# Kernel tuning notes

Hardware: AMD Instinct MI355X
Metric: run time of the kernel (lower is better)

## Reference

```python
import jax, jax.numpy as jnp
import numpy as np
from jax import lax

GEN_POLY = ("1111001", "1011011")  # rate 1/2, constraint length 7 (octal 171/133)


def build_trellis(gen_poly):
    """Feed-forward (non-recursive) convolutional trellis tables.

    State = shift-register contents, most-recent bit is the MSB of the state
    index. Returns int32 tables, each [ns, ni]:
      to_nodes[s, b]        : next state from state s with input bit b
      op_by_fromnode[s, b]  : emitted output-symbol index for (s, b)
      from_nodes[j, m]      : m-th predecessor state of state j
      ip_by_tonode[j, m]    : input bit taken on that predecessor transition
    """
    mu = len(gen_poly[0]) - 1
    ns, ni = 2 ** mu, 2
    g = np.array([[int(c) for c in p] for p in gen_poly])  # [conv_n, mu+1]
    to_nodes = np.zeros((ns, ni), np.int32)
    op_by_fromnode = np.zeros((ns, ni), np.int32)
    from_nodes = np.zeros((ns, ni), np.int32)
    ip_by_tonode = np.zeros((ns, ni), np.int32)
    fill = np.zeros(ns, np.int32)
    for s in range(ns):
        rbits = [(s >> (mu - 1 - j)) & 1 for j in range(mu)]
        for b in range(ni):
            w = np.array([b] + rbits)                 # full window [b, r0..r_{mu-1}]
            obits = (g @ w) % 2                        # output bits, MSB first
            o = int("".join(str(int(x)) for x in obits), 2)
            j = int("".join(str(x) for x in ([b] + rbits[:-1])), 2)
            to_nodes[s, b] = j
            op_by_fromnode[s, b] = o
            from_nodes[j, fill[j]] = s
            ip_by_tonode[j, fill[j]] = b
            fill[j] += 1
    return to_nodes, op_by_fromnode, from_nodes, ip_by_tonode


TO_NODES, OP_BY_FROM, FROM_NODES, IP_BY_TO = build_trellis(GEN_POLY)
CONV_N = len(GEN_POLY)
MU = len(GEN_POLY[0]) - 1
NS = 2 ** MU
NO = 2 ** CONV_N
# output-symbol bit patterns, MSB first, mapped to signs (1-2*bit)
_OP_BITS = np.array([[(o >> (CONV_N - 1 - j)) & 1 for j in range(CONV_N)]
                     for o in range(NO)], np.float32)
OP_SIGN = jnp.asarray(1.0 - 2.0 * _OP_BITS)  # [NO, CONV_N]
IP_SIGN = jnp.asarray([1.0, -1.0])           # sign of input bit b: 1-2b


def setup_inputs() -> dict:
    key = jax.random.key(0)
    k1, k2 = jax.random.split(key)
    B, n = 256, 4096
    T = n // CONV_N  # = k = 2048 info bits
    llr_ch = jax.random.normal(k1, (B, n), dtype=jnp.float32)
    llr_a = jax.random.normal(k2, (B, T), dtype=jnp.float32)
    return {"llr_ch": llr_ch, "llr_a": llr_a}


def _bcjr(llr_ch, llr_a):
    B, n = llr_ch.shape
    T = n // CONV_N
    # branch metrics: bm[t, b, o] = exp(0.5 * sum_j llr[b, t, j] * (1-2*opbit_j(o)))
    llr_r = llr_ch.reshape(B, T, CONV_N)
    bm = jnp.exp(0.5 * jnp.einsum('btj,oj->tbo', llr_r, OP_SIGN))  # [T, B, NO]
    llr_a_t = llr_a.T  # [T, B]

    def gamma_fn(bm_t, la_t):
        # a-priori factor exp(0.5*llr_a*(1-2b)) times channel branch metric
        ap = jnp.exp(0.5 * la_t[:, None, None] * IP_SIGN[None, None, :])  # [B,1,2]
        return ap * bm_t[:, OP_BY_FROM]  # [B, NS, 2]

    alpha0 = jnp.zeros((B, NS), jnp.float32).at[:, 0].set(1.0)

    def fwd(alpha_prev, inp):
        bm_t, la_t = inp
        gam = gamma_fn(bm_t, la_t)                        # [B, NS, 2] by from-state
        ag = gam * alpha_prev[:, :, None]                  # alpha_{t} * gamma_t
        agt = ag[:, FROM_NODES, IP_BY_TO]                  # regroup by to-state
        alpha = agt.sum(-1)
        alpha = alpha / alpha.sum(-1, keepdims=True)       # normalize (as in TF code)
        return alpha, alpha_prev                            # emit alpha BEFORE step t

    _, alphas = lax.scan(fwd, alpha0, (bm, llr_a_t))       # alphas[t] = alpha_t, [T,B,NS]

    beta_T = jnp.full((B, NS), 1.0 / NS, jnp.float32)      # non-terminated: uniform

    def bwd(beta_next, inp):
        bm_t, la_t, alpha_t = inp
        gam = gamma_fn(bm_t, la_t)                         # [B, NS, 2]
        bg = gam * beta_next[:, TO_NODES]                  # gamma * beta_{t+1}(to)
        beta = bg.sum(-1)
        beta = beta / beta.sum(-1, keepdims=True)
        joint = alpha_t[:, :, None] * bg                   # APP per (state, bit)
        llr_t = jnp.log(joint[..., 0].sum(-1)) - jnp.log(joint[..., 1].sum(-1))
        return beta, llr_t

    _, llrs_rev = lax.scan(bwd, beta_T, (bm[::-1], llr_a_t[::-1], alphas[::-1]))
    return llrs_rev[::-1].T  # [B, T] soft LLRs (hard_out=False)


def reference(llr_ch, llr_a):
    return _bcjr(llr_ch, llr_a)
```

## Files before the change

### kernel.cpp

```cpp
#include <hip/hip_runtime.h>

#define T_LEN 2048
#define NSTATE 64
#define NCHUNK 16
#define CH_S 128
#define WARM 64
#define NCH_B 32
#define CH_B 64
#define RK 16

template <int CTRL>
__device__ __forceinline__ float dpp_add(float v) {
    int r = __builtin_amdgcn_update_dpp(0, __float_as_int(v), CTRL, 0xF, 0xF, true);
    return v + __int_as_float(r);
}
__device__ __forceinline__ float red63(float v) {
    v = dpp_add<0x111>(v);
    v = dpp_add<0x112>(v);
    v = dpp_add<0x114>(v);
    v = dpp_add<0x118>(v);
    v = dpp_add<0x142>(v);
    v = dpp_add<0x143>(v);
    return v;
}
__device__ __forceinline__ float red_half(float v) {
    v = dpp_add<0x111>(v);
    v = dpp_add<0x112>(v);
    v = dpp_add<0x114>(v);
    v = dpp_add<0x118>(v);
    v = dpp_add<0x142>(v);
    return v;
}
__device__ __forceinline__ float rdlane(float v, int l) {
    return __uint_as_float(__builtin_amdgcn_readlane(__float_as_uint(v), l));
}
__device__ __forceinline__ float bcast63(float v) { return rdlane(v, 63); }
__device__ __forceinline__ float pair_sum_xor1(float v) { return dpp_add<0xB1>(v); }
__device__ __forceinline__ unsigned short bf16_of(float f) {
    return (unsigned short)((__float_as_uint(f) + 0x8000u) >> 16);
}
__device__ __forceinline__ float bf16_lo(unsigned u) { return __uint_as_float(u << 16); }
__device__ __forceinline__ float bf16_hi(unsigned u) { return __uint_as_float(u & 0xffff0000u); }


__global__ __launch_bounds__(256, 8)
void bcjr_beta_kernel(const float* __restrict__ llr_ch,
                      const float* __restrict__ llr_a,
                      unsigned short* __restrict__ wsB)
{
    const int wave  = blockIdx.x * 4 + (threadIdx.x >> 6);
    const int lane  = threadIdx.x & 63;
    const int chunk = wave & (NCH_B - 1);
    const int b     = wave >> 5;

    const float c0 = 1.0f - 2.0f * (float)(__popc(lane & 57) & 1);
    const float c1 = 1.0f - 2.0f * (float)(__popc(lane & 27) & 1);
    const float kE = 0.5f * 1.442695040888963f;
    const float k0 = kE * c0, k1 = kE * c1;

    const float* chp = llr_ch + (size_t)b * (2 * T_LEN);
    const float* lap = llr_a  + (size_t)b * T_LEN;
    unsigned short* w = wsB + (size_t)b * T_LEN * NSTATE;

    const int bs0 = lane >> 1;
    const int bs1 = 32 + (lane >> 1);
    const int t0 = chunk * CH_B;
    const int te = (chunk == NCH_B - 1) ? (t0 + CH_B) : (t0 + CH_B + WARM);
    float state = 1.0f / 64.0f;

    for (int g = te - RK; g >= t0; g -= RK) {
        const bool store = (g < t0 + CH_B);
        #pragma unroll
        for (int h = 1; h >= 0; --h) {
            const int gb = g + 8 * h;
            const float4* c4 = (const float4*)(chp + 2 * gb);
            const float4* a4 = (const float4*)(lap + gb);
            float4 cc[4], aa[2];
            #pragma unroll
            for (int i = 0; i < 4; ++i) cc[i] = c4[i];
            #pragma unroll
            for (int i = 0; i < 2; ++i) aa[i] = a4[i];
            unsigned short* wb = w + (size_t)gb * NSTATE + lane;
            #pragma unroll
            for (int i = 7; i >= 0; --i) {
                float l0 = (i & 1) ? cc[i >> 1].z : cc[i >> 1].x;
                float l1 = (i & 1) ? cc[i >> 1].w : cc[i >> 1].y;
                float la = ((const float*)aa)[i];
                if (store) wb[i * NSTATE] = bf16_of(state);
                float x   = fmaf(la, kE, fmaf(l0, k0, l1 * k1));
                float g0v = exp2f(x);
                float g1v = __builtin_amdgcn_rcpf(g0v);
                float t0v = __shfl(state, bs0, 64);
                float t1v = __shfl(state, bs1, 64);
                state = fmaf(g0v, t0v, g1v * t1v);
            }
        }
        float s = bcast63(red63(state));
        state = state * __builtin_amdgcn_rcpf(s);
    }
}

__global__ __launch_bounds__(256, 4)
void bcjr_alpha_llr_kernel(const float* __restrict__ llr_ch,
                           const float* __restrict__ llr_a,
                           const unsigned short* __restrict__ wsB,
                           float* __restrict__ out)
{
    const int wave  = blockIdx.x * 4 + (threadIdx.x >> 6);
    const int lane  = threadIdx.x & 63;
    const int chunk = wave & (NCHUNK - 1);
    const int b     = wave >> 4;

    const float c0 = 1.0f - 2.0f * (float)(__popc(lane & 57) & 1);
    const float c1 = 1.0f - 2.0f * (float)(__popc(lane & 27) & 1);
    const float kE = 0.5f * 1.442695040888963f;
    const float k0 = kE * c0, k1 = kE * c1;
    const float LN2 = 0.69314718055994531f;

    const float* chp = llr_ch + (size_t)b * (2 * T_LEN);
    const float* lap = llr_a  + (size_t)b * T_LEN;
    float* outp      = out    + (size_t)b * T_LEN;

    const int  fs0 = 2 * (lane & 31);
    const bool fhi = (lane >= 32);
    const int t0 = chunk * CH_S;
    const int ts = (chunk == 0) ? t0 : t0 - WARM;
    float state = (chunk == 0) ? ((lane == 0) ? 1.0f : 0.0f) : (1.0f / 64.0f);

    for (int g = ts; g < t0; g += RK) {
        #pragma unroll
        for (int h = 0; h < 2; ++h) {
            const int gb = g + 8 * h;
            const float4* c4 = (const float4*)(chp + 2 * gb);
            const float4* a4 = (const float4*)(lap + gb);
            float4 cc[4], aa[2];
            #pragma unroll
            for (int i = 0; i < 4; ++i) cc[i] = c4[i];
            #pragma unroll
            for (int i = 0; i < 2; ++i) aa[i] = a4[i];
            #pragma unroll
            for (int i = 0; i < 8; ++i) {
                float l0 = (i & 1) ? cc[i >> 1].z : cc[i >> 1].x;
                float l1 = (i & 1) ? cc[i >> 1].w : cc[i >> 1].y;
                float la = ((const float*)aa)[i];
                float x   = fmaf(la, kE, fmaf(l0, k0, l1 * k1));
                float g0v = exp2f(x);
                float g1v = __builtin_amdgcn_rcpf(g0v);
                float s0  = pair_sum_xor1(state * g0v);
                float s1  = pair_sum_xor1(state * g1v);
                float a0  = __shfl(s0, fs0, 64);
                float a1  = __shfl(s1, fs0, 64);
                state = fhi ? a1 : a0;
            }
        }
        float s = bcast63(red63(state));
        state = state * __builtin_amdgcn_rcpf(s);
    }

    const unsigned* brow = (const unsigned*)(wsB + (size_t)b * T_LEN * NSTATE);
    const int  bdw = lane >> 1;
    const bool bhi = (lane & 1) != 0;
    float keep = 0.0f;

    for (int g = t0; g < t0 + CH_S; g += RK) {
        #pragma unroll
        for (int h = 0; h < 2; ++h) {
            const int gb = g + 8 * h;
            const float4* c4 = (const float4*)(chp + 2 * gb);
            const float4* a4 = (const float4*)(lap + gb);
            float4 cc[4], aa[2];
            #pragma unroll
            for (int i = 0; i < 4; ++i) cc[i] = c4[i];
            #pragma unroll
            for (int i = 0; i < 2; ++i) aa[i] = a4[i];
            unsigned bu[8];
            const unsigned* r = brow + (size_t)gb * 32;
            #pragma unroll
            for (int i = 0; i < 8; ++i) bu[i] = r[i * 32 + bdw];
            #pragma unroll
            for (int i = 0; i < 8; ++i) {
                const int t = gb + i;
                float l0 = (i & 1) ? cc[i >> 1].z : cc[i >> 1].x;
                float l1 = (i & 1) ? cc[i >> 1].w : cc[i >> 1].y;
                float la = ((const float*)aa)[i];
                float x   = fmaf(la, kE, fmaf(l0, k0, l1 * k1));
                float g0v = exp2f(x);
                float g1v = __builtin_amdgcn_rcpf(g0v);
                float ag0 = state * g0v;
                float ag1 = state * g1v;
                float s0  = pair_sum_xor1(ag0);
                float s1  = pair_sum_xor1(ag1);
                float a0  = __shfl(s0, fs0, 64);
                float a1  = __shfl(s1, fs0, 64);
                float an  = fhi ? a1 : a0;
                float bv  = bhi ? bf16_hi(bu[i]) : bf16_lo(bu[i]);
                float v   = red_half(an * bv);
                float n0  = rdlane(v, 31);
                float n1  = rdlane(v, 63);
                float llr = LN2 * (__log2f(n0) - __log2f(n1));
                keep = (lane == (t & 63)) ? llr : keep;
                state = an;
            }
        }
        if ((g & 63) == 48) outp[g - 48 + lane] = keep;
        float s = bcast63(red63(state));
        state = state * __builtin_amdgcn_rcpf(s);
    }
}

extern "C" void kernel_launch(void* const* d_in, const int* in_sizes, int n_in,
                              void* d_out, int out_size, void* d_ws, size_t ws_size,
                              hipStream_t stream) {
    const float* llr_ch = (const float*)d_in[0];
    const float* llr_a  = (const float*)d_in[1];
    float* out = (float*)d_out;
    unsigned short* wsB = (unsigned short*)d_ws;

    int B = in_sizes[0] / (2 * T_LEN);
    int nw_beta  = B * NCH_B;
    int nw_alpha = B * NCHUNK;
    hipLaunchKernelGGL(bcjr_beta_kernel, dim3(nw_beta / 4), dim3(256), 0, stream,
                       llr_ch, llr_a, wsB);
    hipLaunchKernelGGL(bcjr_alpha_llr_kernel, dim3(nw_alpha / 4), dim3(256), 0, stream,
                       llr_ch, llr_a, wsB, out);
}
```

Before: 142.2 us.

## Fuse beta and alpha/LLR passes into one kernel with beta in LDS

Replaces the two-kernel scheme (a beta pass writing bf16 betas to global workspace, then an alpha+LLR pass reading them back) with a single kernel. Each 128-thread block owns a 128-step chunk: two waves each compute betas for one 64-step half into shared memory, synchronise, then each runs the forward alpha recursion with warm-up and the LLR output for its half. This removes the global round-trip of the beta table and the second launch. The cost is more warm-up recursion per output step on the alpha side, 16 KB of LDS per block, and smaller blocks. The log-ratio is also computed as a single log of a ratio instead of two logs.

```diff
diff --git a/kernel.cpp b/kernel.cpp
--- a/kernel.cpp
+++ b/kernel.cpp
@@ -1,12 +1,10 @@
 #include <hip/hip_runtime.h>
 
 #define T_LEN 2048
-#define NSTATE 64
 #define NCHUNK 16
-#define CH_S 128
+#define CH 128
+#define HALF 64
 #define WARM 64
-#define NCH_B 32
-#define CH_B 64
 #define RK 16
 
 template <int CTRL>
@@ -39,77 +37,20 @@
 __device__ __forceinline__ unsigned short bf16_of(float f) {
     return (unsigned short)((__float_as_uint(f) + 0x8000u) >> 16);
 }
-__device__ __forceinline__ float bf16_lo(unsigned u) { return __uint_as_float(u << 16); }
-__device__ __forceinline__ float bf16_hi(unsigned u) { return __uint_as_float(u & 0xffff0000u); }
-
-
-__global__ __launch_bounds__(256, 8)
-void bcjr_beta_kernel(const float* __restrict__ llr_ch,
-                      const float* __restrict__ llr_a,
-                      unsigned short* __restrict__ wsB)
+
+__global__ __launch_bounds__(128, 5)
+void bcjr_one(const float* __restrict__ llr_ch,
+              const float* __restrict__ llr_a,
+              float* __restrict__ out)
 {
-    const int wave  = blockIdx.x * 4 + (threadIdx.x >> 6);
+    __shared__ unsigned short lds_b[CH * 64];
+
+    const int blk   = blockIdx.x;
+    const int b     = blk >> 4;
+    const int chunk = blk & (NCHUNK - 1);
+    const int wave  = threadIdx.x >> 6;
     const int lane  = threadIdx.x & 63;
-    const int chunk = wave & (NCH_B - 1);
-    const int b     = wave >> 5;
-
-    const float c0 = 1.0f - 2.0f * (float)(__popc(lane & 57) & 1);
-    const float c1 = 1.0f - 2.0f * (float)(__popc(lane & 27) & 1);
-    const float kE = 0.5f * 1.442695040888963f;
-    const float k0 = kE * c0, k1 = kE * c1;
-
-    const float* chp = llr_ch + (size_t)b * (2 * T_LEN);
-    const float* lap = llr_a  + (size_t)b * T_LEN;
-    unsigned short* w = wsB + (size_t)b * T_LEN * NSTATE;
-
-    const int bs0 = lane >> 1;
-    const int bs1 = 32 + (lane >> 1);
-    const int t0 = chunk * CH_B;
-    const int te = (chunk == NCH_B - 1) ? (t0 + CH_B) : (t0 + CH_B + WARM);
-    float state = 1.0f / 64.0f;
-
-    for (int g = te - RK; g >= t0; g -= RK) {
-        const bool store = (g < t0 + CH_B);
-        #pragma unroll
-        for (int h = 1; h >= 0; --h) {
-            const int gb = g + 8 * h;
-            const float4* c4 = (const float4*)(chp + 2 * gb);
-            const float4* a4 = (const float4*)(lap + gb);
-            float4 cc[4], aa[2];
-            #pragma unroll
-            for (int i = 0; i < 4; ++i) cc[i] = c4[i];
-            #pragma unroll
-            for (int i = 0; i < 2; ++i) aa[i] = a4[i];
-            unsigned short* wb = w + (size_t)gb * NSTATE + lane;
-            #pragma unroll
-            for (int i = 7; i >= 0; --i) {
-                float l0 = (i & 1) ? cc[i >> 1].z : cc[i >> 1].x;
-                float l1 = (i & 1) ? cc[i >> 1].w : cc[i >> 1].y;
-                float la = ((const float*)aa)[i];
-                if (store) wb[i * NSTATE] = bf16_of(state);
-                float x   = fmaf(la, kE, fmaf(l0, k0, l1 * k1));
-                float g0v = exp2f(x);
-                float g1v = __builtin_amdgcn_rcpf(g0v);
-                float t0v = __shfl(state, bs0, 64);
-                float t1v = __shfl(state, bs1, 64);
-                state = fmaf(g0v, t0v, g1v * t1v);
-            }
-        }
-        float s = bcast63(red63(state));
-        state = state * __builtin_amdgcn_rcpf(s);
-    }
-}
-
-__global__ __launch_bounds__(256, 4)
-void bcjr_alpha_llr_kernel(const float* __restrict__ llr_ch,
-                           const float* __restrict__ llr_a,
-                           const unsigned short* __restrict__ wsB,
-                           float* __restrict__ out)
-{
-    const int wave  = blockIdx.x * 4 + (threadIdx.x >> 6);
-    const int lane  = threadIdx.x & 63;
-    const int chunk = wave & (NCHUNK - 1);
-    const int b     = wave >> 4;
+    const int t0    = chunk * CH;
 
     const float c0 = 1.0f - 2.0f * (float)(__popc(lane & 57) & 1);
     const float c1 = 1.0f - 2.0f * (float)(__popc(lane & 27) & 1);
@@ -119,92 +60,132 @@
 
     const float* chp = llr_ch + (size_t)b * (2 * T_LEN);
     const float* lap = llr_a  + (size_t)b * T_LEN;
-    float* outp      = out    + (size_t)b * T_LEN;
-
-    const int  fs0 = 2 * (lane & 31);
-    const bool fhi = (lane >= 32);
-    const int t0 = chunk * CH_S;
-    const int ts = (chunk == 0) ? t0 : t0 - WARM;
-    float state = (chunk == 0) ? ((lane == 0) ? 1.0f : 0.0f) : (1.0f / 64.0f);
-
-    for (int g = ts; g < t0; g += RK) {
-        #pragma unroll
-        for (int h = 0; h < 2; ++h) {
-            const int gb = g + 8 * h;
-            const float4* c4 = (const float4*)(chp + 2 * gb);
-            const float4* a4 = (const float4*)(lap + gb);
-            float4 cc[4], aa[2];
+
+    {
+        const int sbeg = wave ? t0 : (t0 + HALF);
+        const int hi = (wave == 0 && chunk == NCHUNK - 1) ? (t0 + CH)
+                                                          : (sbeg + HALF + WARM);
+        const int bs0 = lane >> 1, bs1 = 32 + (lane >> 1);
+        float state = 1.0f / 64.0f;
+
+        for (int g = hi - RK; g >= sbeg; g -= RK) {
             #pragma unroll
-            for (int i = 0; i < 4; ++i) cc[i] = c4[i];
+            for (int h = 1; h >= 0; --h) {
+                const int gb = g + 8 * h;
+                const float4* c4 = (const float4*)(chp + 2 * gb);
+                const float4* a4 = (const float4*)(lap + gb);
+                float4 cc[4], aa[2];
+                #pragma unroll
+                for (int i = 0; i < 4; ++i) cc[i] = c4[i];
+                #pragma unroll
+                for (int i = 0; i < 2; ++i) aa[i] = a4[i];
+                #pragma unroll
+                for (int i = 7; i >= 0; --i) {
+                    const int t = gb + i;
+                    float l0 = (i & 1) ? cc[i >> 1].z : cc[i >> 1].x;
+                    float l1 = (i & 1) ? cc[i >> 1].w : cc[i >> 1].y;
+                    float la = ((const float*)aa)[i];
+                    if (t < sbeg + HALF)
+                        lds_b[(t - t0) * 64 + lane] = bf16_of(state);
+                    float x   = fmaf(la, kE, fmaf(l0, k0, l1 * k1));
+                    float g0v = exp2f(x);
+                    float g1v = __builtin_amdgcn_rcpf(g0v);
+                    float t0v = __shfl(state, bs0, 64);
+                    float t1v = __shfl(state, bs1, 64);
+                    state = fmaf(g0v, t0v, g1v * t1v);
+                }
+            }
+            float s = bcast63(red63(state));
+            state = state * __builtin_amdgcn_rcpf(s);
+        }
+    }
+
+    __syncthreads();
+
+    {
+        const int fbeg = wave ? (t0 + HALF) : t0;
+        int ts = fbeg - WARM;
+        float state;
+        if (ts <= 0) { ts = 0; state = (lane == 0) ? 1.0f : 0.0f; }
+        else         { state = 1.0f / 64.0f; }
+        const int  fs0 = 2 * (lane & 31);
+        const bool fhi = (lane >= 32);
+
+        for (int g = ts; g < fbeg; g += RK) {
             #pragma unroll
-            for (int i = 0; i < 2; ++i) aa[i] = a4[i];
+            for (int h = 0; h < 2; ++h) {
+                const int gb = g + 8 * h;
+                const float4* c4 = (const float4*)(chp + 2 * gb);
+                const float4* a4 = (const float4*)(lap + gb);
+                float4 cc[4], aa[2];
+                #pragma unroll
+                for (int i = 0; i < 4; ++i) cc[i] = c4[i];
+                #pragma unroll
+                for (int i = 0; i < 2; ++i) aa[i] = a4[i];
+                #pragma unroll
+                for (int i = 0; i < 8; ++i) {
+                    float l0 = (i & 1) ? cc[i >> 1].z : cc[i >> 1].x;
+                    float l1 = (i & 1) ? cc[i >> 1].w : cc[i >> 1].y;
+                    float la = ((const float*)aa)[i];
+                    float x   = fmaf(la, kE, fmaf(l0, k0, l1 * k1));
+                    float g0v = exp2f(x);
+                    float g1v = __builtin_amdgcn_rcpf(g0v);
+                    float s0  = pair_sum_xor1(state * g0v);
+                    float s1  = pair_sum_xor1(state * g1v);
+                    float a0  = __shfl(s0, fs0, 64);
+                    float a1  = __shfl(s1, fs0, 64);
+                    state = fhi ? a1 : a0;
+                }
+            }
+            float s = bcast63(red63(state));
+            state = state * __builtin_amdgcn_rcpf(s);
+        }
+
+        float keep = 0.0f;
+        for (int g = fbeg; g < fbeg + HALF; g += RK) {
             #pragma unroll
-            for (int i = 0; i < 8; ++i) {
-                float l0 = (i & 1) ? cc[i >> 1].z : cc[i >> 1].x;
-                float l1 = (i & 1) ? cc[i >> 1].w : cc[i >> 1].y;
-                float la = ((const float*)aa)[i];
-                float x   = fmaf(la, kE, fmaf(l0, k0, l1 * k1));
-                float g0v = exp2f(x);
-                float g1v = __builtin_amdgcn_rcpf(g0v);
-                float s0  = pair_sum_xor1(state * g0v);
-                float s1  = pair_sum_xor1(state * g1v);
-                float a0  = __shfl(s0, fs0, 64);
-                float a1  = __shfl(s1, fs0, 64);
-                state = fhi ? a1 : a0;
+            for (int h = 0; h < 2; ++h) {
+                const int gb = g + 8 * h;
+                const float4* c4 = (const float4*)(chp + 2 * gb);
+                const float4* a4 = (const float4*)(lap + gb);
+                float4 cc[4], aa[2];
+                #pragma unroll
+                for (int i = 0; i < 4; ++i) cc[i] = c4[i];
+                #pragma unroll
+                for (int i = 0; i < 2; ++i) aa[i] = a4[i];
+                unsigned short bu[8];
+                #pragma unroll
+                for (int i = 0; i < 8; ++i)
+                    bu[i] = lds_b[(gb - t0 + i) * 64 + lane];
+                #pragma unroll
+                for (int i = 0; i < 8; ++i) {
+                    const int t = gb + i;
+                    float l0 = (i & 1) ? cc[i >> 1].z : cc[i >> 1].x;
+                    float l1 = (i & 1) ? cc[i >> 1].w : cc[i >> 1].y;
+                    float la = ((const float*)aa)[i];
+                    float x   = fmaf(la, kE, fmaf(l0, k0, l1 * k1));
+                    float g0v = exp2f(x);
+                    float g1v = __builtin_amdgcn_rcpf(g0v);
+                    float ag0 = state * g0v;
+                    float ag1 = state * g1v;
+                    float s0  = pair_sum_xor1(ag0);
+                    float s1  = pair_sum_xor1(ag1);
+                    float a0  = __shfl(s0, fs0, 64);
+                    float a1  = __shfl(s1, fs0, 64);
+                    float an  = fhi ? a1 : a0;
+                    float bv  = __uint_as_float(((unsigned)bu[i]) << 16);
+                    float v   = red_half(an * bv);
+                    float n0  = rdlane(v, 31);
+                    float n1  = rdlane(v, 63);
+                    float llr = LN2 * __log2f(n0 * __builtin_amdgcn_rcpf(n1));
+                    keep = (lane == (t & 63)) ? llr : keep;
+                    state = an;
+                }
             }
+            float s = bcast63(red63(state));
+            state = state * __builtin_amdgcn_rcpf(s);
         }
-        float s = bcast63(red63(state));
-        state = state * __builtin_amdgcn_rcpf(s);
-    }
-
-    const unsigned* brow = (const unsigned*)(wsB + (size_t)b * T_LEN * NSTATE);
-    const int  bdw = lane >> 1;
-    const bool bhi = (lane & 1) != 0;
-    float keep = 0.0f;
-
-    for (int g = t0; g < t0 + CH_S; g += RK) {
-        #pragma unroll
-        for (int h = 0; h < 2; ++h) {
-            const int gb = g + 8 * h;
-            const float4* c4 = (const float4*)(chp + 2 * gb);
-            const float4* a4 = (const float4*)(lap + gb);
-            float4 cc[4], aa[2];
-            #pragma unroll
-            for (int i = 0; i < 4; ++i) cc[i] = c4[i];
-            #pragma unroll
-            for (int i = 0; i < 2; ++i) aa[i] = a4[i];
-            unsigned bu[8];
-            const unsigned* r = brow + (size_t)gb * 32;
-            #pragma unroll
-            for (int i = 0; i < 8; ++i) bu[i] = r[i * 32 + bdw];
-            #pragma unroll
-            for (int i = 0; i < 8; ++i) {
-                const int t = gb + i;
-                float l0 = (i & 1) ? cc[i >> 1].z : cc[i >> 1].x;
-                float l1 = (i & 1) ? cc[i >> 1].w : cc[i >> 1].y;
-                float la = ((const float*)aa)[i];
-                float x   = fmaf(la, kE, fmaf(l0, k0, l1 * k1));
-                float g0v = exp2f(x);
-                float g1v = __builtin_amdgcn_rcpf(g0v);
-                float ag0 = state * g0v;
-                float ag1 = state * g1v;
-                float s0  = pair_sum_xor1(ag0);
-                float s1  = pair_sum_xor1(ag1);
-                float a0  = __shfl(s0, fs0, 64);
-                float a1  = __shfl(s1, fs0, 64);
-                float an  = fhi ? a1 : a0;
-                float bv  = bhi ? bf16_hi(bu[i]) : bf16_lo(bu[i]);
-                float v   = red_half(an * bv);
-                float n0  = rdlane(v, 31);
-                float n1  = rdlane(v, 63);
-                float llr = LN2 * (__log2f(n0) - __log2f(n1));
-                keep = (lane == (t & 63)) ? llr : keep;
-                state = an;
-            }
-        }
-        if ((g & 63) == 48) outp[g - 48 + lane] = keep;
-        float s = bcast63(red63(state));
-        state = state * __builtin_amdgcn_rcpf(s);
+        out[(size_t)b * T_LEN + fbeg + lane] = keep;
     }
 }
 
@@ -214,13 +195,8 @@
     const float* llr_ch = (const float*)d_in[0];
     const float* llr_a  = (const float*)d_in[1];
     float* out = (float*)d_out;
-    unsigned short* wsB = (unsigned short*)d_ws;
 
     int B = in_sizes[0] / (2 * T_LEN);
-    int nw_beta  = B * NCH_B;
-    int nw_alpha = B * NCHUNK;
-    hipLaunchKernelGGL(bcjr_beta_kernel, dim3(nw_beta / 4), dim3(256), 0, stream,
-                       llr_ch, llr_a, wsB);
-    hipLaunchKernelGGL(bcjr_alpha_llr_kernel, dim3(nw_alpha / 4), dim3(256), 0, stream,
-                       llr_ch, llr_a, wsB, out);
-}
+    hipLaunchKernelGGL(bcjr_one, dim3(B * NCHUNK), dim3(128), 0, stream,
+                       llr_ch, llr_a, out);
+}
```

Result: slower. 150.2 us (+5.6%).
